# Kernel optimization log

Measured on AMD Instinct MI355X. Metric: run time of the kernel, lower is better.

## Reference

```python
import jax, jax.numpy as jnp
import numpy as np

HEADS = 16
D_HEAD = 64
EPS = 1e-5


def _ln(x, g, b):
    m = jnp.mean(x, axis=-1, keepdims=True)
    v = jnp.var(x, axis=-1, keepdims=True)
    return (x - m) * jax.lax.rsqrt(v + EPS) * g + b


def _attn(xq, xc, Wq, Wk, Wv, Wo, bo):
    # Wq: [dim, inner], Wk/Wv: [ctx_dim, inner], Wo: [inner, dim]
    B, N, _ = xq.shape
    S = xc.shape[1]
    q = (xq @ Wq).reshape(B, N, HEADS, D_HEAD)
    k = (xc @ Wk).reshape(B, S, HEADS, D_HEAD)
    v = (xc @ Wv).reshape(B, S, HEADS, D_HEAD)
    scale = D_HEAD ** -0.5
    scores = jnp.einsum('bnhd,bshd->bhns', q, k) * scale
    attn = jax.nn.softmax(scores, axis=-1)
    out = jnp.einsum('bhns,bshd->bnhd', attn, v).reshape(B, N, HEADS * D_HEAD)
    return out @ Wo + bo


def _geglu_ff(x, Wp, bp, Wf, bf):
    h = x @ Wp + bp  # [B,N,2*inner]
    a, gate = jnp.split(h, 2, axis=-1)
    # torch F.gelu default is exact (erf) gelu
    return (a * jax.nn.gelu(gate, approximate=False)) @ Wf + bf


def setup_inputs() -> dict:
    key = jax.random.key(0)
    ks = jax.random.split(key, 16)
    dim, ctx, inner, ffin = 1024, 768, HEADS * D_HEAD, 4 * 1024
    def w(k, i, o):
        return jax.random.normal(k, (i, o), jnp.float32) * (i ** -0.5)
    inp = {
        'x': jax.random.normal(ks[0], (4, 2048, dim), jnp.float32),
        'context': jax.random.normal(ks[1], (4, 77, ctx), jnp.float32),
        'Wq1': w(ks[2], dim, inner), 'Wk1': w(ks[3], dim, inner), 'Wv1': w(ks[4], dim, inner),
        'Wo1': w(ks[5], inner, dim), 'bo1': jnp.zeros((dim,), jnp.float32),
        'Wq2': w(ks[6], dim, inner), 'Wk2': w(ks[7], ctx, inner), 'Wv2': w(ks[8], ctx, inner),
        'Wo2': w(ks[9], inner, dim), 'bo2': jnp.zeros((dim,), jnp.float32),
        'Wp': w(ks[10], dim, 2 * ffin), 'bp': jnp.zeros((2 * ffin,), jnp.float32),
        'Wf': w(ks[11], ffin, dim), 'bf': jnp.zeros((dim,), jnp.float32),
        'g1': jnp.ones((dim,), jnp.float32), 'b1': jnp.zeros((dim,), jnp.float32),
        'g2': jnp.ones((dim,), jnp.float32), 'b2': jnp.zeros((dim,), jnp.float32),
        'g3': jnp.ones((dim,), jnp.float32), 'b3': jnp.zeros((dim,), jnp.float32),
    }
    return inp


def reference(x, context, Wq1, Wk1, Wv1, Wo1, bo1, Wq2, Wk2, Wv2, Wo2, bo2,
              Wp, bp, Wf, bf, g1, b1, g2, b2, g3, b3):
    x = _attn(_ln(x, g1, b1), _ln(x, g1, b1), Wq1, Wk1, Wv1, Wo1, bo1) + x
    x = _attn(_ln(x, g2, b2), context, Wq2, Wk2, Wv2, Wo2, bo2) + x
    x = _geglu_ff(_ln(x, g3, b3), Wp, bp, Wf, bf) + x
    return x
```

## Files before the change

### kernel.cpp

```cpp
#include <hip/hip_runtime.h>

typedef unsigned short u16;
typedef __bf16 bf16x8 __attribute__((ext_vector_type(8)));
typedef float f32x4 __attribute__((ext_vector_type(4)));

#define HEADS 16
#define DHEAD 64
#define DIM 1024
#define NTOK 2048
#define BATCH 4
#define CTXD 768
#define SCROSS 77
#define FFIN 4096

__device__ inline float bf2f(u16 v) { return __uint_as_float(((unsigned)v) << 16); }
__device__ inline u16 f2bf(float f) {
    unsigned u = __float_as_uint(f);
    unsigned r = u + 0x7fffu + ((u >> 16) & 1u);
    return (u16)(r >> 16);
}
__device__ inline f32x4 f4zero() { f32x4 v; v[0]=0.f; v[1]=0.f; v[2]=0.f; v[3]=0.f; return v; }
__device__ inline bf16x8 as_bf16x8(uint4 u) { union { uint4 a; bf16x8 b; } c; c.a = u; return c.b; }

__device__ inline void gload_lds16(const u16* g, u16* l) {
    __builtin_amdgcn_global_load_lds((const __attribute__((address_space(1))) unsigned*)g,
                                     (__attribute__((address_space(3))) unsigned*)l, 16, 0, 0);
}

__global__ __launch_bounds__(256) void wt_k(const float* __restrict__ W, u16* __restrict__ WT,
                                            int K, int N, float scale) {
    __shared__ u16 Ts[64][72];
    int k0 = blockIdx.x * 64, n0 = blockIdx.y * 64;
    int t = threadIdx.x;
    int r = t >> 2, c4 = (t & 3) * 16;
    const float* wp = W + (size_t)(k0 + r) * N + n0 + c4;
    #pragma unroll
    for (int j = 0; j < 4; j++) {
        float4 v = *(const float4*)(wp + j * 4);
        Ts[c4 + j * 4 + 0][r] = f2bf(v.x * scale);
        Ts[c4 + j * 4 + 1][r] = f2bf(v.y * scale);
        Ts[c4 + j * 4 + 2][r] = f2bf(v.z * scale);
        Ts[c4 + j * 4 + 3][r] = f2bf(v.w * scale);
    }
    __syncthreads();
    int n = t >> 2, kc = (t & 3) * 16;
    u16* op = WT + (size_t)(n0 + n) * K + k0 + kc;
    *(uint4*)op       = *(const uint4*)&Ts[n][kc];
    *(uint4*)(op + 8) = *(const uint4*)&Ts[n][kc + 8];
}

__global__ __launch_bounds__(256) void cvt_k(const float* __restrict__ X, u16* __restrict__ Y, int n4) {
    int i = blockIdx.x * 256 + threadIdx.x;
    if (i < n4) {
        float4 v = *(const float4*)(X + (size_t)i * 4);
        uint2 o;
        o.x = (unsigned)f2bf(v.x) | ((unsigned)f2bf(v.y) << 16);
        o.y = (unsigned)f2bf(v.z) | ((unsigned)f2bf(v.w) << 16);
        *(uint2*)(Y + (size_t)i * 4) = o;
    }
}

__global__ __launch_bounds__(256) void ln_k(const float* __restrict__ X, const float* __restrict__ G,
                                            const float* __restrict__ Bt, u16* __restrict__ Y) {
    int row = blockIdx.x;
    int t = threadIdx.x;
    int w = t >> 6, lane = t & 63;
    float4 xv = *(const float4*)(X + (size_t)row * DIM + t * 4);
    float s = xv.x + xv.y + xv.z + xv.w;
    float s2 = xv.x*xv.x + xv.y*xv.y + xv.z*xv.z + xv.w*xv.w;
    for (int off = 1; off < 64; off <<= 1) {
        s  += __shfl_xor(s,  off, 64);
        s2 += __shfl_xor(s2, off, 64);
    }
    __shared__ float rs[4], rs2[4];
    if (lane == 0) { rs[w] = s; rs2[w] = s2; }
    __syncthreads();
    float S_ = rs[0] + rs[1] + rs[2] + rs[3];
    float S2_ = rs2[0] + rs2[1] + rs2[2] + rs2[3];
    float mean = S_ * (1.0f / DIM);
    float var = fmaxf(S2_ * (1.0f / DIM) - mean * mean, 0.f);
    float rstd = rsqrtf(var + 1e-5f);
    int col = t * 4;
    float4 g = *(const float4*)(G + col);
    float4 b = *(const float4*)(Bt + col);
    float y0 = (xv.x - mean) * rstd * g.x + b.x;
    float y1 = (xv.y - mean) * rstd * g.y + b.y;
    float y2 = (xv.z - mean) * rstd * g.z + b.z;
    float y3 = (xv.w - mean) * rstd * g.w + b.w;
    uint2 o;
    o.x = (unsigned)f2bf(y0) | ((unsigned)f2bf(y1) << 16);
    o.y = (unsigned)f2bf(y2) | ((unsigned)f2bf(y3) << 16);
    *(uint2*)(Y + (size_t)row * DIM + col) = o;
}

template<typename TC, bool RESID>
__global__ __launch_bounds__(256) void gemm128(const u16* __restrict__ A, int lda,
                                               const u16* __restrict__ BT,
                                               const float* __restrict__ bias, const float* resid,
                                               TC* C, int ldc, int M, int N, int K) {
    __shared__ __align__(16) u16 As[128 * 32];
    __shared__ __align__(16) u16 Bs[128 * 32];
    int m0 = blockIdx.x * 128, n0 = blockIdx.y * 128;
    int t = threadIdx.x;
    int w = t >> 6, lane = t & 63;
    int quad = lane >> 4, l16 = lane & 15;
    int mh = (w & 1) * 64, nh = (w >> 1) * 64;
    f32x4 acc[4][4];
    #pragma unroll
    for (int i = 0; i < 4; i++)
        #pragma unroll
        for (int j = 0; j < 4; j++) acc[i][j] = f4zero();
    int sr = t >> 2;
    int sc8 = (t & 3) * 8;
    int ra0 = min(m0 + sr, M - 1);
    int ra1 = min(m0 + sr + 64, M - 1);
    const u16* ga0 = A + (size_t)ra0 * lda + sc8;
    const u16* ga1 = A + (size_t)ra1 * lda + sc8;
    const u16* gb0 = BT + (size_t)(n0 + sr) * K + sc8;
    const u16* gb1 = BT + (size_t)(n0 + sr + 64) * K + sc8;
    u16* lA0 = &As[w * 512];
    u16* lA1 = &As[2048 + w * 512];
    u16* lB0 = &Bs[w * 512];
    u16* lB1 = &Bs[2048 + w * 512];
    for (int k0 = 0; k0 < K; k0 += 32) {
        __syncthreads();
        gload_lds16(ga0 + k0, lA0);
        gload_lds16(ga1 + k0, lA1);
        gload_lds16(gb0 + k0, lB0);
        gload_lds16(gb1 + k0, lB1);
        __syncthreads();
        bf16x8 af[4], bfv[4];
        #pragma unroll
        for (int i = 0; i < 4; i++) {
            af[i]  = as_bf16x8(*(const uint4*)&As[(mh + i * 16 + l16) * 32 + quad * 8]);
            bfv[i] = as_bf16x8(*(const uint4*)&Bs[(nh + i * 16 + l16) * 32 + quad * 8]);
        }
        #pragma unroll
        for (int i = 0; i < 4; i++)
            #pragma unroll
            for (int j = 0; j < 4; j++)
                acc[i][j] = __builtin_amdgcn_mfma_f32_16x16x32_bf16(af[i], bfv[j], acc[i][j], 0, 0, 0);
    }
    #pragma unroll
    for (int j = 0; j < 4; j++) {
        int gn = n0 + nh + j * 16 + l16;
        float bv = bias ? bias[gn] : 0.f;
        #pragma unroll
        for (int i = 0; i < 4; i++) {
            #pragma unroll
            for (int r = 0; r < 4; r++) {
                int gm = m0 + mh + i * 16 + quad * 4 + r;
                if (gm < M) {
                    float v = acc[i][j][r] + bv;
                    if constexpr (RESID) v += resid[(size_t)gm * N + gn];
                    if constexpr (__is_same(TC, u16)) C[(size_t)gm * ldc + gn] = f2bf(v);
                    else                              C[(size_t)gm * ldc + gn] = v;
                }
            }
        }
    }
}

__global__ __launch_bounds__(256, 2) void gemm_geglu(const u16* __restrict__ A,
                                                     const u16* __restrict__ BT,
                                                     const float* __restrict__ bp,
                                                     u16* __restrict__ Gb, int M) {
    __shared__ __align__(16) u16 As[128 * 32];
    __shared__ __align__(16) u16 Bs1[128 * 32];
    __shared__ __align__(16) u16 Bs2[128 * 32];
    const int K = DIM;
    int m0 = blockIdx.x * 128, n0 = blockIdx.y * 128;
    int t = threadIdx.x;
    int w = t >> 6, lane = t & 63;
    int quad = lane >> 4, l16 = lane & 15;
    int mh = (w & 1) * 64, nh = (w >> 1) * 64;
    f32x4 acc1[4][4], acc2[4][4];
    #pragma unroll
    for (int i = 0; i < 4; i++)
        #pragma unroll
        for (int j = 0; j < 4; j++) { acc1[i][j] = f4zero(); acc2[i][j] = f4zero(); }
    int sr = t >> 2;
    int sc8 = (t & 3) * 8;
    const u16* ga0 = A + (size_t)(m0 + sr) * K + sc8;
    const u16* ga1 = A + (size_t)(m0 + sr + 64) * K + sc8;
    const u16* gb0 = BT + (size_t)(n0 + sr) * K + sc8;
    const u16* gb1 = BT + (size_t)(n0 + sr + 64) * K + sc8;
    const u16* gc0 = BT + (size_t)(FFIN + n0 + sr) * K + sc8;
    const u16* gc1 = BT + (size_t)(FFIN + n0 + sr + 64) * K + sc8;
    u16* lA0 = &As[w * 512];
    u16* lA1 = &As[2048 + w * 512];
    u16* lB0 = &Bs1[w * 512];
    u16* lB1 = &Bs1[2048 + w * 512];
    u16* lC0 = &Bs2[w * 512];
    u16* lC1 = &Bs2[2048 + w * 512];
    for (int k0 = 0; k0 < K; k0 += 32) {
        __syncthreads();
        gload_lds16(ga0 + k0, lA0);
        gload_lds16(ga1 + k0, lA1);
        gload_lds16(gb0 + k0, lB0);
        gload_lds16(gb1 + k0, lB1);
        gload_lds16(gc0 + k0, lC0);
        gload_lds16(gc1 + k0, lC1);
        __syncthreads();
        bf16x8 af[4];
        #pragma unroll
        for (int i = 0; i < 4; i++)
            af[i] = as_bf16x8(*(const uint4*)&As[(mh + i * 16 + l16) * 32 + quad * 8]);
        #pragma unroll
        for (int j = 0; j < 4; j++) {
            bf16x8 b1 = as_bf16x8(*(const uint4*)&Bs1[(nh + j * 16 + l16) * 32 + quad * 8]);
            bf16x8 b2 = as_bf16x8(*(const uint4*)&Bs2[(nh + j * 16 + l16) * 32 + quad * 8]);
            #pragma unroll
            for (int i = 0; i < 4; i++) {
                acc1[i][j] = __builtin_amdgcn_mfma_f32_16x16x32_bf16(af[i], b1, acc1[i][j], 0, 0, 0);
                acc2[i][j] = __builtin_amdgcn_mfma_f32_16x16x32_bf16(af[i], b2, acc2[i][j], 0, 0, 0);
            }
        }
    }
    #pragma unroll
    for (int j = 0; j < 4; j++) {
        int gn = n0 + nh + j * 16 + l16;
        float b1v = bp[gn];
        float b2v = bp[FFIN + gn];
        #pragma unroll
        for (int i = 0; i < 4; i++) {
            #pragma unroll
            for (int r = 0; r < 4; r++) {
                int gm = m0 + mh + i * 16 + quad * 4 + r;
                float a = acc1[i][j][r] + b1v;
                float g = acc2[i][j][r] + b2v;
                float v = a * (0.5f * g * (1.f + erff(g * 0.70710678118654752f)));
                Gb[(size_t)gm * FFIN + gn] = f2bf(v);
            }
        }
    }
}

__global__ __launch_bounds__(256) void attn_k(const u16* Q, int ldq, const u16* __restrict__ K,
                                              const u16* __restrict__ V, int ldkv,
                                              u16* O, int S) {
    __shared__ __align__(16) u16 Ksh[2][4096];
    __shared__ __align__(16) u16 Vt[4][2048];
    __shared__ __align__(16) u16 Pb[4][4][512];
    int bh = blockIdx.x;
    int b = bh >> 4, h = bh & 15;
    int q0 = blockIdx.y * 64;
    int t = threadIdx.x;
    int w = t >> 6, lane = t & 63;
    int quad = lane >> 4, l16 = lane & 15;
    const u16* Qp = Q + ((size_t)b * NTOK + q0) * ldq + h * DHEAD;
    const u16* Kp = K + (size_t)b * S * ldkv + h * DHEAD;
    const u16* Vp = V + (size_t)b * S * ldkv + h * DHEAD;
    bf16x8 qf[2];
    #pragma unroll
    for (int ds = 0; ds < 2; ds++)
        qf[ds] = as_bf16x8(*(const uint4*)(Qp + (size_t)(w * 16 + l16) * ldq + ds * 32 + quad * 8));
    float l_l = 0.f;
    f32x4 o_acc[4];
    #pragma unroll
    for (int dt = 0; dt < 4; dt++) o_acc[dt] = f4zero();
    int cA = w * 128 + lane;
    int krA = cA >> 2, kdA = (cA & 3) * 8;
    int krB = (cA + 64) >> 2, kdB = ((cA + 64) & 3) * 8;
    int vd = (t >> 5) * 8;
    int vk = (t & 31) * 4;
    int vkk = vk >> 5, vcol = vk & 31;
    int nkt = (S + 127) / 128;
    for (int kt = 0; kt < nkt; kt++) {
        int kbase = kt * 128;
        bool full = (kbase + 128) <= S;
        __syncthreads();
        {
            int rA = min(kbase + krA, S - 1);
            int rB = min(kbase + krB, S - 1);
            const u16* kgA = Kp + (size_t)rA * ldkv;
            const u16* kgB = Kp + (size_t)rB * ldkv;
            gload_lds16(kgA + kdA,      &Ksh[0][w * 1024]);
            gload_lds16(kgB + kdB,      &Ksh[0][w * 1024 + 512]);
            gload_lds16(kgA + 32 + kdA, &Ksh[1][w * 1024]);
            gload_lds16(kgB + 32 + kdB, &Ksh[1][w * 1024 + 512]);
        }
        {
            union { uint4 u; u16 e[8]; } vr[4];
            #pragma unroll
            for (int j = 0; j < 4; j++) {
                int key = min(kbase + vk + j, S - 1);
                vr[j].u = *(const uint4*)(Vp + (size_t)key * ldkv + vd);
            }
            #pragma unroll
            for (int d = 0; d < 8; d++) {
                uint2 p;
                p.x = (unsigned)vr[0].e[d] | ((unsigned)vr[1].e[d] << 16);
                p.y = (unsigned)vr[2].e[d] | ((unsigned)vr[3].e[d] << 16);
                *(uint2*)&Vt[vkk][(vd + d) * 32 + vcol] = p;
            }
        }
        __syncthreads();
        f32x4 sc[8];
        #pragma unroll
        for (int sub = 0; sub < 8; sub++) {
            bf16x8 kf0 = as_bf16x8(*(const uint4*)&Ksh[0][(sub * 16 + l16) * 32 + quad * 8]);
            bf16x8 kf1 = as_bf16x8(*(const uint4*)&Ksh[1][(sub * 16 + l16) * 32 + quad * 8]);
            f32x4 s = __builtin_amdgcn_mfma_f32_16x16x32_bf16(kf0, qf[0], f4zero(), 0, 0, 0);
            sc[sub] = __builtin_amdgcn_mfma_f32_16x16x32_bf16(kf1, qf[1], s, 0, 0, 0);
        }
        if (!full) {
            #pragma unroll
            for (int sub = 0; sub < 8; sub++)
                #pragma unroll
                for (int r = 0; r < 4; r++)
                    if (kbase + sub * 16 + quad * 4 + r >= S) sc[sub][r] = -1e30f;
        }
        float psum = 0.f;
        #pragma unroll
        for (int sub = 0; sub < 8; sub++) {
            float p0 = __builtin_amdgcn_exp2f(sc[sub][0]);
            float p1 = __builtin_amdgcn_exp2f(sc[sub][1]);
            float p2 = __builtin_amdgcn_exp2f(sc[sub][2]);
            float p3 = __builtin_amdgcn_exp2f(sc[sub][3]);
            psum += (p0 + p1) + (p2 + p3);
            uint2 pk;
            pk.x = __builtin_amdgcn_perm(__float_as_uint(p1), __float_as_uint(p0), 0x07060302);
            pk.y = __builtin_amdgcn_perm(__float_as_uint(p3), __float_as_uint(p2), 0x07060302);
            *(uint2*)&Pb[w][sub >> 1][l16 * 32 + (sub & 1) * 16 + quad * 4] = pk;
        }
        l_l += psum;
        #pragma unroll
        for (int kk = 0; kk < 4; kk++) {
            bf16x8 pf = as_bf16x8(*(const uint4*)&Pb[w][kk][l16 * 32 + quad * 8]);
            #pragma unroll
            for (int dt = 0; dt < 4; dt++) {
                bf16x8 vf = as_bf16x8(*(const uint4*)&Vt[kk][(dt * 16 + l16) * 32 + quad * 8]);
                o_acc[dt] = __builtin_amdgcn_mfma_f32_16x16x32_bf16(pf, vf, o_acc[dt], 0, 0, 0);
            }
        }
    }
    float l_tot = l_l;
    l_tot += __shfl_xor(l_tot, 16, 64);
    l_tot += __shfl_xor(l_tot, 32, 64);
    #pragma unroll
    for (int r = 0; r < 4; r++) {
        float lr = __shfl(l_tot, quad * 4 + r, 64);
        float invl = (lr > 0.f) ? (1.f / lr) : 0.f;
        int gq = q0 + w * 16 + quad * 4 + r;
        #pragma unroll
        for (int dt = 0; dt < 4; dt++) {
            O[((size_t)b * NTOK + gq) * ldq + h * DHEAD + dt * 16 + l16] = f2bf(o_acc[dt][r] * invl);
        }
    }
}

extern "C" void kernel_launch(void* const* d_in, const int* in_sizes, int n_in,
                              void* d_out, int out_size, void* d_ws, size_t ws_size,
                              hipStream_t stream) {
    const float* x   = (const float*)d_in[0];
    const float* ctx = (const float*)d_in[1];
    const float* Wq1 = (const float*)d_in[2];
    const float* Wk1 = (const float*)d_in[3];
    const float* Wv1 = (const float*)d_in[4];
    const float* Wo1 = (const float*)d_in[5];
    const float* bo1 = (const float*)d_in[6];
    const float* Wq2 = (const float*)d_in[7];
    const float* Wk2 = (const float*)d_in[8];
    const float* Wv2 = (const float*)d_in[9];
    const float* Wo2 = (const float*)d_in[10];
    const float* bo2 = (const float*)d_in[11];
    const float* Wp  = (const float*)d_in[12];
    const float* bp  = (const float*)d_in[13];
    const float* Wf  = (const float*)d_in[14];
    const float* bfb = (const float*)d_in[15];
    const float* g1  = (const float*)d_in[16];
    const float* b1  = (const float*)d_in[17];
    const float* g2  = (const float*)d_in[18];
    const float* b2  = (const float*)d_in[19];
    const float* g3  = (const float*)d_in[20];
    const float* b3  = (const float*)d_in[21];
    float* out = (float*)d_out;

    const int M = BATCH * NTOK;
    const int Mc = BATCH * SCROSS;
    u16* ws = (u16*)d_ws;
    size_t o = 0;
    u16* WqT1 = ws + o; o += (size_t)DIM * DIM;
    u16* WkT1 = ws + o; o += (size_t)DIM * DIM;
    u16* WvT1 = ws + o; o += (size_t)DIM * DIM;
    u16* WoT1 = ws + o; o += (size_t)DIM * DIM;
    u16* WqT2 = ws + o; o += (size_t)DIM * DIM;
    u16* WoT2 = ws + o; o += (size_t)DIM * DIM;
    u16* WkT2 = ws + o; o += (size_t)DIM * CTXD;
    u16* WvT2 = ws + o; o += (size_t)DIM * CTXD;
    u16* WpT  = ws + o; o += (size_t)(2 * FFIN) * DIM;
    u16* WfT  = ws + o; o += (size_t)DIM * FFIN;
    u16* ctxb = ws + o; o += (size_t)Mc * CTXD;
    u16* KVc  = ws + o; o += (size_t)Mc * 2048;
    u16* P    = ws + o; o += (size_t)M * DIM;
    u16* QKV  = ws + o; o += (size_t)M * 3072;
    u16* reg2 = ws + o; o += (size_t)M * DIM * 2;
    float* X1 = (float*)reg2;
    u16* gb = QKV;

    dim3 blk(256);
    const float qscale = 0.125f * 1.4426950408889634f;

    wt_k<<<dim3(16, 16), blk, 0, stream>>>(Wq1, WqT1, DIM, DIM, qscale);
    wt_k<<<dim3(16, 16), blk, 0, stream>>>(Wk1, WkT1, DIM, DIM, 1.f);
    wt_k<<<dim3(16, 16), blk, 0, stream>>>(Wv1, WvT1, DIM, DIM, 1.f);
    wt_k<<<dim3(16, 16), blk, 0, stream>>>(Wo1, WoT1, DIM, DIM, 1.f);
    wt_k<<<dim3(16, 16), blk, 0, stream>>>(Wq2, WqT2, DIM, DIM, qscale);
    wt_k<<<dim3(16, 16), blk, 0, stream>>>(Wo2, WoT2, DIM, DIM, 1.f);
    wt_k<<<dim3(12, 16), blk, 0, stream>>>(Wk2, WkT2, CTXD, DIM, 1.f);
    wt_k<<<dim3(12, 16), blk, 0, stream>>>(Wv2, WvT2, CTXD, DIM, 1.f);
    wt_k<<<dim3(16, 128), blk, 0, stream>>>(Wp, WpT, DIM, 2 * FFIN, 1.f);
    wt_k<<<dim3(64, 16), blk, 0, stream>>>(Wf, WfT, FFIN, DIM, 1.f);
    cvt_k<<<dim3((Mc * CTXD / 4 + 255) / 256), blk, 0, stream>>>(ctx, ctxb, Mc * CTXD / 4);

    ln_k<<<dim3(M), blk, 0, stream>>>(x, g1, b1, P);
    gemm128<u16, false><<<dim3(M / 128, 3072 / 128), blk, 0, stream>>>(
        P, DIM, WqT1, nullptr, nullptr, QKV, 3072, M, 3072, DIM);
    attn_k<<<dim3(BATCH * HEADS, NTOK / 64), blk, 0, stream>>>(
        QKV, 3072, QKV + 1024, QKV + 2048, 3072, QKV, NTOK);
    gemm128<float, true><<<dim3(M / 128, DIM / 128), blk, 0, stream>>>(
        QKV, 3072, WoT1, bo1, x, X1, DIM, M, DIM, DIM);

    ln_k<<<dim3(M), blk, 0, stream>>>(X1, g2, b2, P);
    gemm128<u16, false><<<dim3(M / 128, DIM / 128), blk, 0, stream>>>(
        P, DIM, WqT2, nullptr, nullptr, QKV, 3072, M, DIM, DIM);
    gemm128<u16, false><<<dim3((Mc + 127) / 128, 2048 / 128), blk, 0, stream>>>(
        ctxb, CTXD, WkT2, nullptr, nullptr, KVc, 2048, Mc, 2048, CTXD);
    attn_k<<<dim3(BATCH * HEADS, NTOK / 64), blk, 0, stream>>>(
        QKV, 3072, KVc, KVc + 1024, 2048, QKV, SCROSS);
    gemm128<float, true><<<dim3(M / 128, DIM / 128), blk, 0, stream>>>(
        QKV, 3072, WoT2, bo2, X1, out, DIM, M, DIM, DIM);

    ln_k<<<dim3(M), blk, 0, stream>>>(out, g3, b3, P);
    gemm_geglu<<<dim3(M / 128, FFIN / 128), blk, 0, stream>>>(P, WpT, bp, gb, M);
    gemm128<float, true><<<dim3(M / 128, DIM / 128), blk, 0, stream>>>(
        gb, FFIN, WfT, bfb, out, out, DIM, M, DIM, FFIN);
}
```

Baseline: 945.1 us.

## Swizzle LDS layouts, interleave GEGLU weights, add setprio and V prefetch

Applies XOR swizzling to LDS tiles in the GEMM and attention kernels so fragment reads avoid bank conflicts. The Wp transpose now interleaves value and gate columns in 16-wide groups, which lets the GEGLU GEMM run as a plain 128x128 tile with half the accumulators and twice the grid. The MFMA loops are wrapped in s_setprio, and the attention kernel prefetches the next V tile into registers and uses a single 64-wide K tile layout. These changes lower register pressure and LDS conflicts, but they change occupancy and add index arithmetic.

```diff
diff --git a/kernel.cpp b/kernel.cpp
--- a/kernel.cpp
+++ b/kernel.cpp
@@ -27,8 +27,11 @@
                                      (__attribute__((address_space(3))) unsigned*)l, 16, 0, 0);
 }
 
+#define PRIO1() __builtin_amdgcn_s_setprio(1)
+#define PRIO0() __builtin_amdgcn_s_setprio(0)
+
 __global__ __launch_bounds__(256) void wt_k(const float* __restrict__ W, u16* __restrict__ WT,
-                                            int K, int N, float scale) {
+                                            int K, int N, float scale, int remap) {
     __shared__ u16 Ts[64][72];
     int k0 = blockIdx.x * 64, n0 = blockIdx.y * 64;
     int t = threadIdx.x;
@@ -44,7 +47,9 @@
     }
     __syncthreads();
     int n = t >> 2, kc = (t & 3) * 16;
-    u16* op = WT + (size_t)(n0 + n) * K + k0 + kc;
+    int ng = n0 + n;
+    if (remap) ng = ((ng & 4095) >> 4) * 32 + ((ng >> 12) << 4) + (ng & 15);
+    u16* op = WT + (size_t)ng * K + k0 + kc;
     *(uint4*)op       = *(const uint4*)&Ts[n][kc];
     *(uint4*)(op + 8) = *(const uint4*)&Ts[n][kc + 8];
 }
@@ -111,7 +116,7 @@
         #pragma unroll
         for (int j = 0; j < 4; j++) acc[i][j] = f4zero();
     int sr = t >> 2;
-    int sc8 = (t & 3) * 8;
+    int sc8 = (((t & 3) ^ ((sr >> 1) & 3)) * 8);
     int ra0 = min(m0 + sr, M - 1);
     int ra1 = min(m0 + sr + 64, M - 1);
     const u16* ga0 = A + (size_t)ra0 * lda + sc8;
@@ -122,6 +127,7 @@
     u16* lA1 = &As[2048 + w * 512];
     u16* lB0 = &Bs[w * 512];
     u16* lB1 = &Bs[2048 + w * 512];
+    int rq = ((quad ^ ((l16 >> 1) & 3)) * 8);
     for (int k0 = 0; k0 < K; k0 += 32) {
         __syncthreads();
         gload_lds16(ga0 + k0, lA0);
@@ -132,14 +138,16 @@
         bf16x8 af[4], bfv[4];
         #pragma unroll
         for (int i = 0; i < 4; i++) {
-            af[i]  = as_bf16x8(*(const uint4*)&As[(mh + i * 16 + l16) * 32 + quad * 8]);
-            bfv[i] = as_bf16x8(*(const uint4*)&Bs[(nh + i * 16 + l16) * 32 + quad * 8]);
-        }
+            af[i]  = as_bf16x8(*(const uint4*)&As[(mh + i * 16 + l16) * 32 + rq]);
+            bfv[i] = as_bf16x8(*(const uint4*)&Bs[(nh + i * 16 + l16) * 32 + rq]);
+        }
+        PRIO1();
         #pragma unroll
         for (int i = 0; i < 4; i++)
             #pragma unroll
             for (int j = 0; j < 4; j++)
                 acc[i][j] = __builtin_amdgcn_mfma_f32_16x16x32_bf16(af[i], bfv[j], acc[i][j], 0, 0, 0);
+        PRIO0();
     }
     #pragma unroll
     for (int j = 0; j < 4; j++) {
@@ -161,76 +169,70 @@
     }
 }
 
-__global__ __launch_bounds__(256, 2) void gemm_geglu(const u16* __restrict__ A,
+__global__ __launch_bounds__(256) void gemm128_geglu(const u16* __restrict__ A,
                                                      const u16* __restrict__ BT,
                                                      const float* __restrict__ bp,
-                                                     u16* __restrict__ Gb, int M) {
+                                                     u16* __restrict__ C) {
+    const int K = DIM;
     __shared__ __align__(16) u16 As[128 * 32];
-    __shared__ __align__(16) u16 Bs1[128 * 32];
-    __shared__ __align__(16) u16 Bs2[128 * 32];
-    const int K = DIM;
+    __shared__ __align__(16) u16 Bs[128 * 32];
     int m0 = blockIdx.x * 128, n0 = blockIdx.y * 128;
     int t = threadIdx.x;
     int w = t >> 6, lane = t & 63;
     int quad = lane >> 4, l16 = lane & 15;
     int mh = (w & 1) * 64, nh = (w >> 1) * 64;
-    f32x4 acc1[4][4], acc2[4][4];
+    f32x4 acc[4][4];
     #pragma unroll
     for (int i = 0; i < 4; i++)
         #pragma unroll
-        for (int j = 0; j < 4; j++) { acc1[i][j] = f4zero(); acc2[i][j] = f4zero(); }
+        for (int j = 0; j < 4; j++) acc[i][j] = f4zero();
     int sr = t >> 2;
-    int sc8 = (t & 3) * 8;
+    int sc8 = (((t & 3) ^ ((sr >> 1) & 3)) * 8);
     const u16* ga0 = A + (size_t)(m0 + sr) * K + sc8;
     const u16* ga1 = A + (size_t)(m0 + sr + 64) * K + sc8;
     const u16* gb0 = BT + (size_t)(n0 + sr) * K + sc8;
     const u16* gb1 = BT + (size_t)(n0 + sr + 64) * K + sc8;
-    const u16* gc0 = BT + (size_t)(FFIN + n0 + sr) * K + sc8;
-    const u16* gc1 = BT + (size_t)(FFIN + n0 + sr + 64) * K + sc8;
     u16* lA0 = &As[w * 512];
     u16* lA1 = &As[2048 + w * 512];
-    u16* lB0 = &Bs1[w * 512];
-    u16* lB1 = &Bs1[2048 + w * 512];
-    u16* lC0 = &Bs2[w * 512];
-    u16* lC1 = &Bs2[2048 + w * 512];
+    u16* lB0 = &Bs[w * 512];
+    u16* lB1 = &Bs[2048 + w * 512];
+    int rq = ((quad ^ ((l16 >> 1) & 3)) * 8);
     for (int k0 = 0; k0 < K; k0 += 32) {
         __syncthreads();
         gload_lds16(ga0 + k0, lA0);
         gload_lds16(ga1 + k0, lA1);
         gload_lds16(gb0 + k0, lB0);
         gload_lds16(gb1 + k0, lB1);
-        gload_lds16(gc0 + k0, lC0);
-        gload_lds16(gc1 + k0, lC1);
-        __syncthreads();
-        bf16x8 af[4];
+        __syncthreads();
+        bf16x8 af[4], bfv[4];
+        #pragma unroll
+        for (int i = 0; i < 4; i++) {
+            af[i]  = as_bf16x8(*(const uint4*)&As[(mh + i * 16 + l16) * 32 + rq]);
+            bfv[i] = as_bf16x8(*(const uint4*)&Bs[(nh + i * 16 + l16) * 32 + rq]);
+        }
+        PRIO1();
         #pragma unroll
         for (int i = 0; i < 4; i++)
-            af[i] = as_bf16x8(*(const uint4*)&As[(mh + i * 16 + l16) * 32 + quad * 8]);
-        #pragma unroll
-        for (int j = 0; j < 4; j++) {
-            bf16x8 b1 = as_bf16x8(*(const uint4*)&Bs1[(nh + j * 16 + l16) * 32 + quad * 8]);
-            bf16x8 b2 = as_bf16x8(*(const uint4*)&Bs2[(nh + j * 16 + l16) * 32 + quad * 8]);
-            #pragma unroll
-            for (int i = 0; i < 4; i++) {
-                acc1[i][j] = __builtin_amdgcn_mfma_f32_16x16x32_bf16(af[i], b1, acc1[i][j], 0, 0, 0);
-                acc2[i][j] = __builtin_amdgcn_mfma_f32_16x16x32_bf16(af[i], b2, acc2[i][j], 0, 0, 0);
-            }
-        }
-    }
-    #pragma unroll
-    for (int j = 0; j < 4; j++) {
-        int gn = n0 + nh + j * 16 + l16;
-        float b1v = bp[gn];
-        float b2v = bp[FFIN + gn];
+            #pragma unroll
+            for (int j = 0; j < 4; j++)
+                acc[i][j] = __builtin_amdgcn_mfma_f32_16x16x32_bf16(af[i], bfv[j], acc[i][j], 0, 0, 0);
+        PRIO0();
+    }
+    int oc0 = ((n0 + nh) >> 1) + l16;
+    #pragma unroll
+    for (int jp = 0; jp < 2; jp++) {
+        int oc = oc0 + jp * 16;
+        float ba = bp[oc];
+        float bg = bp[FFIN + oc];
         #pragma unroll
         for (int i = 0; i < 4; i++) {
             #pragma unroll
             for (int r = 0; r < 4; r++) {
                 int gm = m0 + mh + i * 16 + quad * 4 + r;
-                float a = acc1[i][j][r] + b1v;
-                float g = acc2[i][j][r] + b2v;
+                float a = acc[i][2 * jp][r] + ba;
+                float g = acc[i][2 * jp + 1][r] + bg;
                 float v = a * (0.5f * g * (1.f + erff(g * 0.70710678118654752f)));
-                Gb[(size_t)gm * FFIN + gn] = f2bf(v);
+                C[(size_t)gm * FFIN + oc] = f2bf(v);
             }
         }
     }
@@ -239,15 +241,16 @@
 __global__ __launch_bounds__(256) void attn_k(const u16* Q, int ldq, const u16* __restrict__ K,
                                               const u16* __restrict__ V, int ldkv,
                                               u16* O, int S) {
-    __shared__ __align__(16) u16 Ksh[2][4096];
-    __shared__ __align__(16) u16 Vt[4][2048];
-    __shared__ __align__(16) u16 Pb[4][4][512];
+    __shared__ __align__(16) u16 Ksh[128 * 64];
+    __shared__ __align__(16) u16 Vt[64 * 128];
+    __shared__ __align__(16) u16 Pb[4][16 * 128];
     int bh = blockIdx.x;
     int b = bh >> 4, h = bh & 15;
     int q0 = blockIdx.y * 64;
     int t = threadIdx.x;
     int w = t >> 6, lane = t & 63;
     int quad = lane >> 4, l16 = lane & 15;
+    int sw = (l16 & 7) << 3;
     const u16* Qp = Q + ((size_t)b * NTOK + q0) * ldq + h * DHEAD;
     const u16* Kp = K + (size_t)b * S * ldkv + h * DHEAD;
     const u16* Vp = V + (size_t)b * S * ldkv + h * DHEAD;
@@ -259,50 +262,53 @@
     f32x4 o_acc[4];
     #pragma unroll
     for (int dt = 0; dt < 4; dt++) o_acc[dt] = f4zero();
-    int cA = w * 128 + lane;
-    int krA = cA >> 2, kdA = (cA & 3) * 8;
-    int krB = (cA + 64) >> 2, kdB = ((cA + 64) & 3) * 8;
+    int kr8 = lane >> 3;
+    int ksl = ((lane & 7) ^ kr8) * 8;
     int vd = (t >> 5) * 8;
     int vk = (t & 31) * 4;
-    int vkk = vk >> 5, vcol = vk & 31;
     int nkt = (S + 127) / 128;
+    union V4 { uint4 u; u16 e[8]; };
+    V4 vrC[4], vrN[4];
+    #pragma unroll
+    for (int j = 0; j < 4; j++) {
+        int key = min(vk + j, S - 1);
+        vrC[j].u = *(const uint4*)(Vp + (size_t)key * ldkv + vd);
+    }
     for (int kt = 0; kt < nkt; kt++) {
         int kbase = kt * 128;
         bool full = (kbase + 128) <= S;
         __syncthreads();
-        {
-            int rA = min(kbase + krA, S - 1);
-            int rB = min(kbase + krB, S - 1);
-            const u16* kgA = Kp + (size_t)rA * ldkv;
-            const u16* kgB = Kp + (size_t)rB * ldkv;
-            gload_lds16(kgA + kdA,      &Ksh[0][w * 1024]);
-            gload_lds16(kgB + kdB,      &Ksh[0][w * 1024 + 512]);
-            gload_lds16(kgA + 32 + kdA, &Ksh[1][w * 1024]);
-            gload_lds16(kgB + 32 + kdB, &Ksh[1][w * 1024 + 512]);
-        }
-        {
-            union { uint4 u; u16 e[8]; } vr[4];
-            #pragma unroll
-            for (int j = 0; j < 4; j++) {
-                int key = min(kbase + vk + j, S - 1);
-                vr[j].u = *(const uint4*)(Vp + (size_t)key * ldkv + vd);
-            }
-            #pragma unroll
-            for (int d = 0; d < 8; d++) {
-                uint2 p;
-                p.x = (unsigned)vr[0].e[d] | ((unsigned)vr[1].e[d] << 16);
-                p.y = (unsigned)vr[2].e[d] | ((unsigned)vr[3].e[d] << 16);
-                *(uint2*)&Vt[vkk][(vd + d) * 32 + vcol] = p;
-            }
+        #pragma unroll
+        for (int i = 0; i < 4; i++) {
+            int r = min(kbase + (i * 4 + w) * 8 + kr8, S - 1);
+            gload_lds16(Kp + (size_t)r * ldkv + ksl, &Ksh[(i * 4 + w) * 512]);
+        }
+        #pragma unroll
+        for (int d = 0; d < 8; d++) {
+            int row = vd + d;
+            uint2 p;
+            p.x = (unsigned)vrC[0].e[d] | ((unsigned)vrC[1].e[d] << 16);
+            p.y = (unsigned)vrC[2].e[d] | ((unsigned)vrC[3].e[d] << 16);
+            *(uint2*)&Vt[row * 128 + (vk ^ ((row & 7) << 3))] = p;
         }
         __syncthreads();
         f32x4 sc[8];
+        PRIO1();
         #pragma unroll
         for (int sub = 0; sub < 8; sub++) {
-            bf16x8 kf0 = as_bf16x8(*(const uint4*)&Ksh[0][(sub * 16 + l16) * 32 + quad * 8]);
-            bf16x8 kf1 = as_bf16x8(*(const uint4*)&Ksh[1][(sub * 16 + l16) * 32 + quad * 8]);
+            const u16* kr = &Ksh[(sub * 16 + l16) * 64];
+            bf16x8 kf0 = as_bf16x8(*(const uint4*)(kr + ((quad * 8) ^ sw)));
+            bf16x8 kf1 = as_bf16x8(*(const uint4*)(kr + ((32 + quad * 8) ^ sw)));
             f32x4 s = __builtin_amdgcn_mfma_f32_16x16x32_bf16(kf0, qf[0], f4zero(), 0, 0, 0);
             sc[sub] = __builtin_amdgcn_mfma_f32_16x16x32_bf16(kf1, qf[1], s, 0, 0, 0);
+        }
+        PRIO0();
+        if (kt + 1 < nkt) {
+            #pragma unroll
+            for (int j = 0; j < 4; j++) {
+                int key = min(kbase + 128 + vk + j, S - 1);
+                vrN[j].u = *(const uint4*)(Vp + (size_t)key * ldkv + vd);
+            }
         }
         if (!full) {
             #pragma unroll
@@ -322,18 +328,22 @@
             uint2 pk;
             pk.x = __builtin_amdgcn_perm(__float_as_uint(p1), __float_as_uint(p0), 0x07060302);
             pk.y = __builtin_amdgcn_perm(__float_as_uint(p3), __float_as_uint(p2), 0x07060302);
-            *(uint2*)&Pb[w][sub >> 1][l16 * 32 + (sub & 1) * 16 + quad * 4] = pk;
+            *(uint2*)&Pb[w][l16 * 128 + ((sub * 16 + quad * 4) ^ sw)] = pk;
         }
         l_l += psum;
+        PRIO1();
         #pragma unroll
         for (int kk = 0; kk < 4; kk++) {
-            bf16x8 pf = as_bf16x8(*(const uint4*)&Pb[w][kk][l16 * 32 + quad * 8]);
+            bf16x8 pf = as_bf16x8(*(const uint4*)&Pb[w][l16 * 128 + ((kk * 32 + quad * 8) ^ sw)]);
             #pragma unroll
             for (int dt = 0; dt < 4; dt++) {
-                bf16x8 vf = as_bf16x8(*(const uint4*)&Vt[kk][(dt * 16 + l16) * 32 + quad * 8]);
+                bf16x8 vf = as_bf16x8(*(const uint4*)&Vt[(dt * 16 + l16) * 128 + ((kk * 32 + quad * 8) ^ sw)]);
                 o_acc[dt] = __builtin_amdgcn_mfma_f32_16x16x32_bf16(pf, vf, o_acc[dt], 0, 0, 0);
             }
         }
+        PRIO0();
+        #pragma unroll
+        for (int j = 0; j < 4; j++) vrC[j] = vrN[j];
     }
     float l_tot = l_l;
     l_tot += __shfl_xor(l_tot, 16, 64);
@@ -402,16 +412,16 @@
     dim3 blk(256);
     const float qscale = 0.125f * 1.4426950408889634f;
 
-    wt_k<<<dim3(16, 16), blk, 0, stream>>>(Wq1, WqT1, DIM, DIM, qscale);
-    wt_k<<<dim3(16, 16), blk, 0, stream>>>(Wk1, WkT1, DIM, DIM, 1.f);
-    wt_k<<<dim3(16, 16), blk, 0, stream>>>(Wv1, WvT1, DIM, DIM, 1.f);
-    wt_k<<<dim3(16, 16), blk, 0, stream>>>(Wo1, WoT1, DIM, DIM, 1.f);
-    wt_k<<<dim3(16, 16), blk, 0, stream>>>(Wq2, WqT2, DIM, DIM, qscale);
-    wt_k<<<dim3(16, 16), blk, 0, stream>>>(Wo2, WoT2, DIM, DIM, 1.f);
-    wt_k<<<dim3(12, 16), blk, 0, stream>>>(Wk2, WkT2, CTXD, DIM, 1.f);
-    wt_k<<<dim3(12, 16), blk, 0, stream>>>(Wv2, WvT2, CTXD, DIM, 1.f);
-    wt_k<<<dim3(16, 128), blk, 0, stream>>>(Wp, WpT, DIM, 2 * FFIN, 1.f);
-    wt_k<<<dim3(64, 16), blk, 0, stream>>>(Wf, WfT, FFIN, DIM, 1.f);
+    wt_k<<<dim3(16, 16), blk, 0, stream>>>(Wq1, WqT1, DIM, DIM, qscale, 0);
+    wt_k<<<dim3(16, 16), blk, 0, stream>>>(Wk1, WkT1, DIM, DIM, 1.f, 0);
+    wt_k<<<dim3(16, 16), blk, 0, stream>>>(Wv1, WvT1, DIM, DIM, 1.f, 0);
+    wt_k<<<dim3(16, 16), blk, 0, stream>>>(Wo1, WoT1, DIM, DIM, 1.f, 0);
+    wt_k<<<dim3(16, 16), blk, 0, stream>>>(Wq2, WqT2, DIM, DIM, qscale, 0);
+    wt_k<<<dim3(16, 16), blk, 0, stream>>>(Wo2, WoT2, DIM, DIM, 1.f, 0);
+    wt_k<<<dim3(12, 16), blk, 0, stream>>>(Wk2, WkT2, CTXD, DIM, 1.f, 0);
+    wt_k<<<dim3(12, 16), blk, 0, stream>>>(Wv2, WvT2, CTXD, DIM, 1.f, 0);
+    wt_k<<<dim3(16, 128), blk, 0, stream>>>(Wp, WpT, DIM, 2 * FFIN, 1.f, 1);
+    wt_k<<<dim3(64, 16), blk, 0, stream>>>(Wf, WfT, FFIN, DIM, 1.f, 0);
     cvt_k<<<dim3((Mc * CTXD / 4 + 255) / 256), blk, 0, stream>>>(ctx, ctxb, Mc * CTXD / 4);
 
     ln_k<<<dim3(M), blk, 0, stream>>>(x, g1, b1, P);
@@ -433,7 +443,7 @@
         QKV, 3072, WoT2, bo2, X1, out, DIM, M, DIM, DIM);
 
     ln_k<<<dim3(M), blk, 0, stream>>>(out, g3, b3, P);
-    gemm_geglu<<<dim3(M / 128, FFIN / 128), blk, 0, stream>>>(P, WpT, bp, gb, M);
+    gemm128_geglu<<<dim3(M / 128, (2 * FFIN) / 128), blk, 0, stream>>>(P, WpT, bp, gb);
     gemm128<float, true><<<dim3(M / 128, DIM / 128), blk, 0, stream>>>(
         gb, FFIN, WfT, bfb, out, out, DIM, M, DIM, FFIN);
 }
```

After: 886.5 us. 1.07x faster.
